# Kernel optimization log

Hardware: AMD Instinct MI355X
Metric: run time of the kernel (lower is better)

Reference implementation:

```python
import jax, jax.numpy as jnp
import numpy as np

D_MODEL = 1024
D_STATE = 16
LN_EPS = 1e-5


def setup_inputs() -> dict:
    key = jax.random.key(0)
    ks = jax.random.split(key, 8)
    batch, seq_len = 8, 4096
    x = jax.random.normal(ks[0], (batch, seq_len, D_MODEL), dtype=jnp.float32)
    A = jax.random.normal(ks[1], (D_STATE, D_STATE), dtype=jnp.float32) * 0.01
    # nn.Linear default init: U(-1/sqrt(fan_in), 1/sqrt(fan_in))
    bb = 1.0 / np.sqrt(D_MODEL)
    B_w = jax.random.uniform(ks[2], (D_STATE, D_MODEL), minval=-bb, maxval=bb)
    B_b = jax.random.uniform(ks[3], (D_STATE,), minval=-bb, maxval=bb)
    cb = 1.0 / np.sqrt(D_STATE)
    C_w = jax.random.uniform(ks[4], (D_MODEL, D_STATE), minval=-cb, maxval=cb)
    C_b = jax.random.uniform(ks[5], (D_MODEL,), minval=-cb, maxval=cb)
    D = jnp.ones((D_MODEL,), dtype=jnp.float32) * 0.01
    gate_w = jax.random.uniform(ks[6], (D_MODEL, D_MODEL), minval=-bb, maxval=bb)
    gate_b = jax.random.uniform(ks[7], (D_MODEL,), minval=-bb, maxval=bb)
    ln_g = jnp.ones((D_MODEL,), dtype=jnp.float32)
    ln_b = jnp.zeros((D_MODEL,), dtype=jnp.float32)
    return {"x": x, "A": A, "B_w": B_w, "B_b": B_b, "C_w": C_w, "C_b": C_b,
            "D": D, "gate_w": gate_w, "gate_b": gate_b, "ln_g": ln_g, "ln_b": ln_b}


def _layer_norm(z, g, b):
    mu = jnp.mean(z, axis=-1, keepdims=True)
    var = jnp.mean(jnp.square(z - mu), axis=-1, keepdims=True)
    return (z - mu) * jax.lax.rsqrt(var + LN_EPS) * g + b


def reference(x, A, B_w, B_b, C_w, C_b, D, gate_w, gate_b, ln_g, ln_b):
    batch, seq_len, d_model = x.shape
    # Precompute B(x_t) for all t in one GEMM: [b, s, d_state]
    Bx = jnp.einsum('bsd,nd->bsn', x, B_w) + B_b

    def step(state, bx_t):  # state: [b, d_state], bx_t: [b, d_state]
        new_state = jnp.tanh(state @ A.T + bx_t)
        return new_state, new_state

    init = jnp.zeros((batch, A.shape[0]), dtype=x.dtype)
    _, states = jax.lax.scan(step, init, jnp.swapaxes(Bx, 0, 1))  # [s, b, n]
    states = jnp.swapaxes(states, 0, 1)  # [b, s, d_state]

    output = jnp.einsum('bsn,dn->bsd', states, C_w) + C_b + D * x
    gate = jax.nn.silu(jnp.einsum('bsd,ed->bse', x, gate_w) + gate_b)
    output = gate * output + (1.0 - gate) * x
    return _layer_norm(output + x, ln_g, ln_b)
```

## Files before the change

### kernel.cpp

```cpp
#include <hip/hip_runtime.h>
#include <hip/hip_bf16.h>
#include <cstdint>
#include <cstddef>

#define DM     1024
#define DSTATE 16
#define SEQ    4096
#define BATCH  8
#define MROWS  (BATCH * SEQ)
#define LNEPS  1e-5f

#define CHUNK  64
#define WARM   16
#define NCHUNK (SEQ / CHUNK)

typedef __hip_bfloat16 bf16;
typedef __attribute__((ext_vector_type(8))) short short8;
typedef __attribute__((ext_vector_type(4))) float f32x4;

static __device__ __forceinline__ unsigned short f2bf(float f) {
  bf16 h = __float2bfloat16(f);
  return __builtin_bit_cast(unsigned short, h);
}

#define GLDS16(SRC, DSTOFF, LDSBASE)                                          \
  __builtin_amdgcn_global_load_lds(                                           \
      (const __attribute__((address_space(1))) void*)(SRC),                   \
      (__attribute__((address_space(3))) void*)((LDSBASE) + (DSTOFF)), 16, 0, 0)

__global__ __launch_bounds__(256) void canon_x(const float* __restrict__ xin,
                                               bf16* __restrict__ wsx) {
  size_t i = ((size_t)blockIdx.x * 256 + threadIdx.x) * 8;
  const float4* p = (const float4*)(xin + i);
  float4 a = p[0], b = p[1];
  uint4 o;
  o.x = (unsigned)f2bf(a.x) | ((unsigned)f2bf(a.y) << 16);
  o.y = (unsigned)f2bf(a.z) | ((unsigned)f2bf(a.w) << 16);
  o.z = (unsigned)f2bf(b.x) | ((unsigned)f2bf(b.y) << 16);
  o.w = (unsigned)f2bf(b.z) | ((unsigned)f2bf(b.w) << 16);
  *(uint4*)(wsx + i) = o;
}

__global__ __launch_bounds__(256) void canon_gw(const float* __restrict__ gw,
                                                bf16* __restrict__ gwc) {
  size_t i = ((size_t)blockIdx.x * 256 + threadIdx.x) * 8;
  const float4* p = (const float4*)(gw + i);
  float4 a = p[0], b = p[1];
  uint4 o;
  o.x = (unsigned)f2bf(a.x) | ((unsigned)f2bf(a.y) << 16);
  o.y = (unsigned)f2bf(a.z) | ((unsigned)f2bf(a.w) << 16);
  o.z = (unsigned)f2bf(b.x) | ((unsigned)f2bf(b.y) << 16);
  o.w = (unsigned)f2bf(b.z) | ((unsigned)f2bf(b.w) << 16);
  *(uint4*)(gwc + i) = o;
}

__global__ __launch_bounds__(256) void bx_kernel(const bf16* __restrict__ X,
                                                 const float* __restrict__ Bw,
                                                 const float* __restrict__ Bb,
                                                 float* __restrict__ Bx) {
  __shared__ __align__(16) char lds[40960];
  const int tid  = threadIdx.x;
  const int lane = tid & 63;
  const int w    = tid >> 6;
  const int fm   = lane & 15;
  const int fq   = lane >> 4;
  const int l4   = lane >> 2, lk = lane & 3;
  const int m0   = blockIdx.x * 64;

  {
    int t6   = tid & 63;
    int nb   = tid >> 6;
    int step = t6 >> 1;
    int cq0  = (t6 & 1) * 2;
#pragma unroll
    for (int p = 0; p < 4; ++p) {
      int n = p * 4 + nb;
      const float4* src = (const float4*)(Bw + (size_t)n * DM + t6 * 16);
      float4 a = src[0], b = src[1], c = src[2], d = src[3];
      uint4 o0, o1;
      o0.x = (unsigned)f2bf(a.x) | ((unsigned)f2bf(a.y) << 16);
      o0.y = (unsigned)f2bf(a.z) | ((unsigned)f2bf(a.w) << 16);
      o0.z = (unsigned)f2bf(b.x) | ((unsigned)f2bf(b.y) << 16);
      o0.w = (unsigned)f2bf(b.z) | ((unsigned)f2bf(b.w) << 16);
      o1.x = (unsigned)f2bf(c.x) | ((unsigned)f2bf(c.y) << 16);
      o1.y = (unsigned)f2bf(c.z) | ((unsigned)f2bf(c.w) << 16);
      o1.z = (unsigned)f2bf(d.x) | ((unsigned)f2bf(d.y) << 16);
      o1.w = (unsigned)f2bf(d.z) | ((unsigned)f2bf(d.w) << 16);
      int sw = (n >> 1) & 3;
      *(uint4*)(lds + step * 1024 + n * 64 + ((cq0 ^ sw) << 4))       = o0;
      *(uint4*)(lds + step * 1024 + n * 64 + (((cq0 + 1) ^ sw) << 4)) = o1;
    }
  }

  const int rowA = w * 16 + l4;
  const int kqA  = lk ^ ((rowA >> 1) & 3);
  GLDS16(X + (size_t)(m0 + rowA) * DM + kqA * 8, 32768 + w * 1024, lds);
  __syncthreads();

  const int rA   = w * 16 + fm;
  const int offA = rA * 64 + ((fq ^ ((rA >> 1) & 3)) << 4);
  const int offB = fm * 64 + ((fq ^ ((fm >> 1) & 3)) << 4);

  f32x4 acc = (f32x4)(0.f);
  for (int t = 0; t < 32; ++t) {
    const int cb = 32768 + (t & 1) * 4096;
    const int sb = 32768 + 4096 - (t & 1) * 4096;
    if (t < 31)
      GLDS16(X + (size_t)(m0 + rowA) * DM + (t + 1) * 32 + kqA * 8,
             sb + w * 1024, lds);
    short8 af  = *(const short8*)(lds + cb + offA);
    short8 bfv = *(const short8*)(lds + t * 1024 + offB);
    acc = __builtin_amdgcn_mfma_f32_16x16x32_bf16(af, bfv, acc, 0, 0, 0);
    __syncthreads();
  }
  float bb = Bb[fm];
#pragma unroll
  for (int q = 0; q < 4; ++q) {
    int row = m0 + w * 16 + fq * 4 + q;
    Bx[(size_t)row * DSTATE + fm] = acc[q] + bb;
  }
}

__global__ __launch_bounds__(64) void scan_kernel(const float* __restrict__ A,
                                                  const float* __restrict__ Bx,
                                                  float* __restrict__ st) {
  int lane = threadIdx.x;
  int n    = lane & 15;
  int base = lane & 48;
  int chain = blockIdx.x * 4 + (lane >> 4);
  int c = chain >> 3;
  int b = chain & 7;

  float Arow[16];
#pragma unroll
  for (int m = 0; m < 16; m++) Arow[m] = A[n * 16 + m];

  int t0   = (c == 0) ? 0 : c * CHUNK - WARM;
  int t1   = c * CHUNK;
  int tEnd = c * CHUNK + CHUNK;

  const float* bxp = Bx + (size_t)b * SEQ * DSTATE + n;
  float*       stp = st + (size_t)b * SEQ * DSTATE + n;

  float state = 0.f;
  for (int t = t0; t < tEnd; t++) {
    float a = bxp[(size_t)t * DSTATE];
#pragma unroll
    for (int m = 0; m < 16; m++)
      a += Arow[m] * __shfl(state, base + m, 64);
    state = tanhf(a);
    if (t >= t1) stp[(size_t)t * DSTATE] = state;
  }
}

#define FBM 32
#define FBK 32
#define NT  (DM / FBK)
#define BUFB 67584
#define CW_OFF 0
#define ST_OFF 65536
#define PART_OFF 67584
#define TOT_OFF 69632
#define BOUNCE 71680

__global__ __launch_bounds__(512, 2) void fused_kernel(
    const bf16* __restrict__ X, const bf16* __restrict__ Gw,
    const float* __restrict__ xf, const float* __restrict__ st,
    const float* __restrict__ Cw, const float* __restrict__ Cb,
    const float* __restrict__ Dv, const float* __restrict__ gb,
    const float* __restrict__ lng, const float* __restrict__ lnb,
    float* __restrict__ out) {
  __shared__ __align__(16) char lds[137216];
  const int tid  = threadIdx.x;
  const int lane = tid & 63;
  const int w    = tid >> 6;
  const int fm   = lane & 15;
  const int fq   = lane >> 4;
  const int m0   = blockIdx.x * FBM;
  const int l4   = lane >> 2, lk = lane & 3;

  int colS[8], kqS[8];
#pragma unroll
  for (int s = 0; s < 8; s++) {
    int col = (w * 8 + s) * 16 + l4;
    colS[s] = col;
    kqS[s]  = lk ^ ((col >> 1) & 3);
  }
  const int rowA = w * 16 + l4;
  const int kqA  = lk ^ ((rowA >> 1) & 3);

  int offA[2], offB[8];
#pragma unroll
  for (int i = 0; i < 2; i++) {
    int r = i * 16 + fm;
    offA[i] = r * 64 + ((fq ^ ((r >> 1) & 3)) << 4);
  }
#pragma unroll
  for (int j = 0; j < 8; j++) {
    int c = w * 128 + j * 16 + fm;
    offB[j] = 2048 + c * 64 + ((fq ^ ((c >> 1) & 3)) << 4);
  }

  f32x4 acc[2][8];
#pragma unroll
  for (int i = 0; i < 2; i++)
#pragma unroll
    for (int j = 0; j < 8; j++) acc[i][j] = (f32x4)(0.f);

  {
#pragma unroll
    for (int s = 0; s < 8; s++)
      GLDS16(Gw + (size_t)colS[s] * DM + kqS[s] * 8,
             2048 + (w * 8 + s) * 1024, lds);
    if (w < 2)
      GLDS16(X + (size_t)(m0 + rowA) * DM + kqA * 8, w * 1024, lds);
  }
  __syncthreads();

  for (int t = 0; t < NT; t++) {
    const int cb = (t & 1) * BUFB;
    const int sb = BUFB - cb;
    if (t < NT - 1) {
      const int kb = (t + 1) * FBK;
#pragma unroll
      for (int s = 0; s < 8; s++)
        GLDS16(Gw + (size_t)colS[s] * DM + kb + kqS[s] * 8,
               sb + 2048 + (w * 8 + s) * 1024, lds);
      if (w < 2)
        GLDS16(X + (size_t)(m0 + rowA) * DM + kb + kqA * 8, sb + w * 1024, lds);
    } else {
#pragma unroll
      for (int s = 0; s < 8; s++) {
        int c   = w * 8 + s;
        int col = c * 16 + l4;
        int nq  = lk ^ ((col >> 1) & 3);
        GLDS16(Cw + (size_t)col * DSTATE + nq * 4, CW_OFF + c * 1024, lds);
      }
      if (w >= 6) {
        int cc  = w - 6;
        int row = cc * 16 + l4;
        int nq  = lk ^ ((row >> 1) & 3);
        GLDS16(st + (size_t)(m0 + row) * DSTATE + nq * 4, ST_OFF + cc * 1024, lds);
      }
    }

    short8 af[2];
#pragma unroll
    for (int i = 0; i < 2; i++) af[i] = *(const short8*)(lds + cb + offA[i]);
#pragma unroll
    for (int j = 0; j < 8; j++) {
      short8 bfj = *(const short8*)(lds + cb + offB[j]);
#pragma unroll
      for (int i = 0; i < 2; i++)
        acc[i][j] = __builtin_amdgcn_mfma_f32_16x16x32_bf16(af[i], bfj,
                                                            acc[i][j], 0, 0, 0);
    }
    __syncthreads();
  }

#pragma unroll
  for (int i = 0; i < 2; i++) {
    f32x4 stv[4][4];
#pragma unroll
    for (int nq = 0; nq < 4; nq++)
#pragma unroll
      for (int r = 0; r < 4; r++) {
        int row = i * 16 + fq * 4 + r;
        stv[nq][r] = *(const f32x4*)(lds + ST_OFF + row * 64 +
                                     ((nq ^ ((row >> 1) & 3)) << 4));
      }
    float sum4[4] = {0.f, 0.f, 0.f, 0.f};
    float ssq4[4] = {0.f, 0.f, 0.f, 0.f};
#pragma unroll
    for (int j = 0; j < 8; j++) {
      int c = w * 128 + j * 16 + fm;
      float oc[4] = {0.f, 0.f, 0.f, 0.f};
#pragma unroll
      for (int nq = 0; nq < 4; nq++) {
        f32x4 cw = *(const f32x4*)(lds + CW_OFF + c * 64 +
                                   ((nq ^ ((c >> 1) & 3)) << 4));
#pragma unroll
        for (int r = 0; r < 4; r++)
          oc[r] += stv[nq][r][0] * cw[0] + stv[nq][r][1] * cw[1] +
                   stv[nq][r][2] * cw[2] + stv[nq][r][3] * cw[3];
      }
      float gbv = gb[c], cbv = Cb[c], dvv = Dv[c];
#pragma unroll
      for (int r = 0; r < 4; r++) {
        int   grow = m0 + i * 16 + fq * 4 + r;
        float xv = xf[(size_t)grow * DM + c];
        float zg = acc[i][j][r] + gbv;
        float g  = zg / (1.f + __expf(-zg));
        float ocf = oc[r] + cbv + dvv * xv;
        float y  = g * ocf + (1.f - g) * xv;
        float z2 = y + xv;
        acc[i][j][r] = z2;
        sum4[r] += z2;
        ssq4[r] += z2 * z2;
      }
    }
#pragma unroll
    for (int r = 0; r < 4; r++) {
#pragma unroll
      for (int off = 1; off < 16; off <<= 1) {
        sum4[r] += __shfl_xor(sum4[r], off, 64);
        ssq4[r] += __shfl_xor(ssq4[r], off, 64);
      }
    }
    if (fm == 0) {
#pragma unroll
      for (int r = 0; r < 4; r++) {
        int row = i * 16 + fq * 4 + r;
        *(float2*)(lds + PART_OFF + w * 256 + row * 8) =
            make_float2(sum4[r], ssq4[r]);
      }
    }
  }
  __syncthreads();

  if (tid < 32) {
    float s = 0.f, q = 0.f;
#pragma unroll
    for (int ww = 0; ww < 8; ww++) {
      float2 p = *(const float2*)(lds + PART_OFF + ww * 256 + tid * 8);
      s += p.x; q += p.y;
    }
    float mu  = s * (1.f / DM);
    float var = q * (1.f / DM) - mu * mu;
    *(float2*)(lds + TOT_OFF + tid * 8) = make_float2(mu, rsqrtf(var + LNEPS));
  }
  __syncthreads();

  for (int h = 0; h < 2; ++h) {
#pragma unroll
    for (int j = 0; j < 8; ++j) {
      int c = w * 128 + j * 16 + fm;
#pragma unroll
      for (int r = 0; r < 4; ++r) {
        int row16 = fq * 4 + r;
        *(float*)(lds + BOUNCE + row16 * 4096 + c * 4) = acc[h][j][r];
      }
    }
    __syncthreads();
    {
      int row16 = tid >> 5;
      int lbase = (tid & 31) * 4;
      float2 mi = *(const float2*)(lds + TOT_OFF + (h * 16 + row16) * 8);
#pragma unroll
      for (int q = 0; q < 8; ++q) {
        int col = lbase + q * 128;
        f32x4 z = *(const f32x4*)(lds + BOUNCE + row16 * 4096 + col * 4);
        float4 g4 = *(const float4*)(lng + col);
        float4 b4 = *(const float4*)(lnb + col);
        float4 ov;
        ov.x = (z[0] - mi.x) * mi.y * g4.x + b4.x;
        ov.y = (z[1] - mi.x) * mi.y * g4.y + b4.y;
        ov.z = (z[2] - mi.x) * mi.y * g4.z + b4.z;
        ov.w = (z[3] - mi.x) * mi.y * g4.w + b4.w;
        *(float4*)(out + (size_t)(m0 + h * 16 + row16) * DM + col) = ov;
      }
    }
    __syncthreads();
  }
}

extern "C" void kernel_launch(void* const* d_in, const int* in_sizes, int n_in,
                              void* d_out, int out_size, void* d_ws, size_t ws_size,
                              hipStream_t stream) {
  (void)in_sizes; (void)n_in;
  const float* x   = (const float*)d_in[0];
  const float* A   = (const float*)d_in[1];
  const float* Bw  = (const float*)d_in[2];
  const float* Bb  = (const float*)d_in[3];
  const float* Cw  = (const float*)d_in[4];
  const float* Cb  = (const float*)d_in[5];
  const float* Dv  = (const float*)d_in[6];
  const float* Gw  = (const float*)d_in[7];
  const float* gb  = (const float*)d_in[8];
  const float* lng = (const float*)d_in[9];
  const float* lnb = (const float*)d_in[10];
  float* out = (float*)d_out;

  const size_t NEED = (size_t)72 << 20;
  if (ws_size < NEED) {
    hipMemsetAsync(d_out, 0, (size_t)out_size * 4, stream);
    return;
  }

  char* ws = (char*)d_ws;
  bf16*  wsx = (bf16*)(ws);
  bf16*  gwc = (bf16*)(ws + ((size_t)64 << 20));
  float* Bx  = (float*)(ws + ((size_t)66 << 20));
  float* st  = (float*)(ws + ((size_t)68 << 20));

  canon_x <<<MROWS * DM / (256 * 8), 256, 0, stream>>>(x, wsx);
  canon_gw<<<DM * DM / (256 * 8), 256, 0, stream>>>(Gw, gwc);
  bx_kernel<<<MROWS / 64, 256, 0, stream>>>(wsx, Bw, Bb, Bx);
  scan_kernel<<<(BATCH * NCHUNK) / 4, 64, 0, stream>>>(A, Bx, st);
  fused_kernel<<<MROWS / FBM, 512, 0, stream>>>(
      wsx, gwc, x, st, Cw, Cb, Dv, gb, lng, lnb, out);
}
```

Baseline: 523.6 us.

## Load GEMM operands directly into registers and use fast exp-based tanh

Result: slower. 635.1 us (+21.3%).

```diff
diff --git a/kernel.cpp b/kernel.cpp
--- a/kernel.cpp
+++ b/kernel.cpp
@@ -148,15 +148,14 @@
 #pragma unroll
     for (int m = 0; m < 16; m++)
       a += Arow[m] * __shfl(state, base + m, 64);
-    state = tanhf(a);
+    float e = __expf(-2.f * fabsf(a));
+    float r = (1.f - e) / (1.f + e);
+    state = __builtin_copysignf(r, a);
     if (t >= t1) stp[(size_t)t * DSTATE] = state;
   }
 }
 
 #define FBM 32
-#define FBK 32
-#define NT  (DM / FBK)
-#define BUFB 67584
 #define CW_OFF 0
 #define ST_OFF 65536
 #define PART_OFF 67584
@@ -179,27 +178,8 @@
   const int m0   = blockIdx.x * FBM;
   const int l4   = lane >> 2, lk = lane & 3;
 
-  int colS[8], kqS[8];
-#pragma unroll
-  for (int s = 0; s < 8; s++) {
-    int col = (w * 8 + s) * 16 + l4;
-    colS[s] = col;
-    kqS[s]  = lk ^ ((col >> 1) & 3);
-  }
-  const int rowA = w * 16 + l4;
-  const int kqA  = lk ^ ((rowA >> 1) & 3);
-
-  int offA[2], offB[8];
-#pragma unroll
-  for (int i = 0; i < 2; i++) {
-    int r = i * 16 + fm;
-    offA[i] = r * 64 + ((fq ^ ((r >> 1) & 3)) << 4);
-  }
-#pragma unroll
-  for (int j = 0; j < 8; j++) {
-    int c = w * 128 + j * 16 + fm;
-    offB[j] = 2048 + c * 64 + ((fq ^ ((c >> 1) & 3)) << 4);
-  }
+  const bf16* aBase = X  + (size_t)(m0 + fm) * DM + fq * 8;
+  const bf16* bBase = Gw + (size_t)(w * 128 + fm) * DM + fq * 8;
 
   f32x4 acc[2][8];
 #pragma unroll
@@ -207,56 +187,49 @@
 #pragma unroll
     for (int j = 0; j < 8; j++) acc[i][j] = (f32x4)(0.f);
 
+#define LOADT(AA, BB, T)                                                      \
+  do {                                                                        \
+    _Pragma("unroll") for (int i = 0; i < 2; i++)                             \
+      AA[i] = *(const short8*)(aBase + (size_t)i * 16 * DM + (T) * 32);       \
+    _Pragma("unroll") for (int j = 0; j < 8; j++)                             \
+      BB[j] = *(const short8*)(bBase + (size_t)j * 16 * DM + (T) * 32);       \
+  } while (0)
+#define MFMAT(AA, BB)                                                         \
+  do {                                                                        \
+    _Pragma("unroll") for (int j = 0; j < 8; j++)                             \
+      _Pragma("unroll") for (int i = 0; i < 2; i++)                           \
+        acc[i][j] = __builtin_amdgcn_mfma_f32_16x16x32_bf16(AA[i], BB[j],     \
+                                                            acc[i][j], 0, 0, 0); \
+  } while (0)
+
   {
-#pragma unroll
-    for (int s = 0; s < 8; s++)
-      GLDS16(Gw + (size_t)colS[s] * DM + kqS[s] * 8,
-             2048 + (w * 8 + s) * 1024, lds);
-    if (w < 2)
-      GLDS16(X + (size_t)(m0 + rowA) * DM + kqA * 8, w * 1024, lds);
+    short8 a0[2], b0[8], a1[2], b1[8];
+    LOADT(a0, b0, 0);
+    for (int t = 0; t < 32; t += 2) {
+      LOADT(a1, b1, t + 1);
+      MFMAT(a0, b0);
+      if (t + 2 < 32) LOADT(a0, b0, t + 2);
+      MFMAT(a1, b1);
+    }
+  }
+#undef LOADT
+#undef MFMAT
+
+  {
+#pragma unroll
+    for (int s = 0; s < 8; s++) {
+      int c   = w * 8 + s;
+      int col = c * 16 + l4;
+      int nq  = lk ^ ((col >> 1) & 3);
+      GLDS16(Cw + (size_t)col * DSTATE + nq * 4, CW_OFF + c * 1024, lds);
+    }
+    if (w < 2) {
+      int row = w * 16 + l4;
+      int nq  = lk ^ ((row >> 1) & 3);
+      GLDS16(st + (size_t)(m0 + row) * DSTATE + nq * 4, ST_OFF + w * 1024, lds);
+    }
   }
   __syncthreads();
-
-  for (int t = 0; t < NT; t++) {
-    const int cb = (t & 1) * BUFB;
-    const int sb = BUFB - cb;
-    if (t < NT - 1) {
-      const int kb = (t + 1) * FBK;
-#pragma unroll
-      for (int s = 0; s < 8; s++)
-        GLDS16(Gw + (size_t)colS[s] * DM + kb + kqS[s] * 8,
-               sb + 2048 + (w * 8 + s) * 1024, lds);
-      if (w < 2)
-        GLDS16(X + (size_t)(m0 + rowA) * DM + kb + kqA * 8, sb + w * 1024, lds);
-    } else {
-#pragma unroll
-      for (int s = 0; s < 8; s++) {
-        int c   = w * 8 + s;
-        int col = c * 16 + l4;
-        int nq  = lk ^ ((col >> 1) & 3);
-        GLDS16(Cw + (size_t)col * DSTATE + nq * 4, CW_OFF + c * 1024, lds);
-      }
-      if (w >= 6) {
-        int cc  = w - 6;
-        int row = cc * 16 + l4;
-        int nq  = lk ^ ((row >> 1) & 3);
-        GLDS16(st + (size_t)(m0 + row) * DSTATE + nq * 4, ST_OFF + cc * 1024, lds);
-      }
-    }
-
-    short8 af[2];
-#pragma unroll
-    for (int i = 0; i < 2; i++) af[i] = *(const short8*)(lds + cb + offA[i]);
-#pragma unroll
-    for (int j = 0; j < 8; j++) {
-      short8 bfj = *(const short8*)(lds + cb + offB[j]);
-#pragma unroll
-      for (int i = 0; i < 2; i++)
-        acc[i][j] = __builtin_amdgcn_mfma_f32_16x16x32_bf16(af[i], bfj,
-                                                            acc[i][j], 0, 0, 0);
-    }
-    __syncthreads();
-  }
 
 #pragma unroll
   for (int i = 0; i < 2; i++) {
```
